# Kernel optimization log

Hardware: AMD Instinct MI355X
Metric: run time of the kernel (lower is better)

## Reference

```python
import jax, jax.numpy as jnp
import numpy as np

S0, S1 = 256, 256          # spins (up, down)
N = S0 + S1                # total electrons
SINGLE = 256               # single_dim == single_out (residual requires match)
PAIR = 128                 # pair_dim == pair_out
GAIN_TANH = 1.5927812698663017  # ActivationWithGain: 1/std(tanh(N(0,1)))
SQRT2 = 1.4142135623730951


def setup_inputs() -> dict:
    key = jax.random.key(0)
    ks = jax.random.split(key, 7)
    h_one = jax.random.normal(ks[0], (N, SINGLE), jnp.float32)
    h_two = jax.random.normal(ks[1], (N, N, PAIR), jnp.float32)
    din = SINGLE + 2 * PAIR  # one_in feature dim = 512
    # variance_scaling(2, fan_in) kernels; bias ~ Normal(0, sqrt(2))
    W1 = jax.random.normal(ks[2], (din, SINGLE), jnp.float32) * (2.0 / din) ** 0.5
    b1 = jax.random.normal(ks[3], (SINGLE,), jnp.float32) * SQRT2
    Wg = jax.random.normal(ks[4], (2 * SINGLE, SINGLE), jnp.float32) * (2.0 / (2 * SINGLE)) ** 0.5
    W2 = jax.random.normal(ks[5], (PAIR, PAIR), jnp.float32) * (2.0 / PAIR) ** 0.5
    b2 = jax.random.normal(ks[6], (PAIR,), jnp.float32) * SQRT2
    return dict(h_one=h_one, h_two=h_two, W1=W1, b1=b1, Wg=Wg, W2=W2, b2=b2)


def _act(x):
    # ActivationWithGain(tanh): rescale so output variance ~ input variance
    return jnp.tanh(x) * jnp.asarray(GAIN_TANH, x.dtype)


def reference(h_one, h_two, W1, b1, Wg, W2, b2):
    # construct_single_features: per-spin mean of h_two over sender axis
    g2_up = jnp.mean(h_two[:S0], axis=0)            # (N, PAIR)
    g2_dn = jnp.mean(h_two[S0:], axis=0)            # (N, PAIR)
    one_in = jnp.concatenate([h_one, g2_up, g2_dn], axis=1)   # (N, SINGLE+2*PAIR)
    # construct_global_features: per-spin mean of h_one, concat on features
    g1_up = jnp.mean(h_one[:S0], axis=0, keepdims=True)       # (1, SINGLE)
    g1_dn = jnp.mean(h_one[S0:], axis=0, keepdims=True)       # (1, SINGLE)
    global_in = jnp.concatenate([g1_up, g1_dn], axis=-1)      # (1, 2*SINGLE)

    h_one_new = one_in @ W1 + b1 + global_in @ Wg             # (N, SINGLE)
    h_one_new = _act(h_one_new / SQRT2)
    h_one_out = (h_one + h_one_new) / SQRT2                   # residual (shapes match)

    h_two_new = _act(h_two @ W2 + b2)                         # (N, N, PAIR)
    h_two_out = (h_two + h_two_new) / SQRT2                   # residual
    return h_one_out, h_two_out
```

## Files before the change

kernel.cpp:

```cpp
#include <hip/hip_runtime.h>
#include <stdint.h>

#define NN 512
#define PAIR 128
#define SINGLE 256

#define GAINv 1.5927812698663017f
#define RS2 0.70710678118654752f

typedef unsigned int uint;
typedef unsigned short ushort;
typedef short bf16x8 __attribute__((ext_vector_type(8)));
typedef float f32x4 __attribute__((ext_vector_type(4)));

__device__ __forceinline__ ushort f2b(float f){
  union{float f;uint i;}v; v.f=f;
  uint x=v.i;
  return (ushort)((x + 0x7FFFu + ((x>>16)&1u))>>16);
}
__device__ __forceinline__ float b2f_lo(uint u){ union{uint i;float f;}v; v.i=u<<16; return v.f; }
__device__ __forceinline__ float b2f_hi(uint u){ union{uint i;float f;}v; v.i=u&0xFFFF0000u; return v.f; }
__device__ __forceinline__ float tanh_fast(float x){
  float xc = fminf(fmaxf(x,-8.f),8.f);
  float e = __expf(2.f*xc);
  return (e-1.f)*__builtin_amdgcn_rcpf(e+1.f);
}

__global__ __launch_bounds__(256) void k1_prep(const float* __restrict__ h_one,
                                               const float* __restrict__ w2,
                                               float* __restrict__ g1part,
                                               ushort* __restrict__ wt,
                                               float* __restrict__ g2acc)
{
  const int b = blockIdx.x, t = threadIdx.x;
  if(b < 8){
    const int rb = b*64;
    float s = 0.f;
    for(int i=0;i<64;i++) s += h_one[(size_t)(rb+i)*SINGLE + t];
    g1part[b*SINGLE + t] = s;
  } else if(b < 16){
    const int bb = b-8;
    for(int e=t; e<16*128; e+=256){
      int kl = e>>7, n = e&127;
      int k = bb*16 + kl;
      wt[n*128 + k] = f2b(w2[(size_t)k*128 + n]);
    }
  } else {
    f32x4 z = (f32x4){0.f,0.f,0.f,0.f};
    f32x4* dst = (f32x4*)g2acc + (size_t)(b-16)*4096;
    for(int q=t; q<4096; q+=256) dst[q] = z;
  }
}

__global__ __launch_bounds__(256) void k2_gterm(const float* __restrict__ g1part,
                                                const float* __restrict__ wg,
                                                float* __restrict__ gtermpart)
{
  __shared__ float g1m[512];
  const int t = threadIdx.x;
  g1m[t]     = (g1part[t]      + g1part[256+t]  + g1part[512+t]  + g1part[768+t])  * (1.f/256.f);
  g1m[t+256] = (g1part[1024+t] + g1part[1280+t] + g1part[1536+t] + g1part[1792+t]) * (1.f/256.f);
  __syncthreads();
  const int fb = blockIdx.x*64;
  float s = 0.f;
  for(int f=fb; f<fb+64; f++)
    s += g1m[f]*wg[(size_t)f*SINGLE + t];
  gtermpart[blockIdx.x*SINGLE + t] = s;
}

__global__ __launch_bounds__(256, 8) void k3_htwo(
    const float* __restrict__ h_two,
    const float* __restrict__ b2,
    const ushort* __restrict__ wt,
    float* __restrict__ g2acc,
    float* __restrict__ out_h2)
{
  __shared__ __align__(16) ushort At[64*128];
  const int tid = threadIdx.x;
  const int w = tid>>6, lane = tid&63;
  const int lq = lane>>4, lr = lane&15;
  const int bi = blockIdx.x & 31, bj = blockIdx.x >> 5;
  const int i0 = bi*16, j0 = bj*4;
  const int spin = bi>>4;

  #pragma unroll
  for(int rep=0;rep<8;rep++){
    const int e = rep*1024 + tid*4;
    const int di = e>>9, c = e&511;
    const float4 v = *(const float4*)(h_two + ((size_t)(i0+di)*NN + j0)*PAIR + c);
    ushort4 pk; pk.x=f2b(v.x); pk.y=f2b(v.y); pk.z=f2b(v.z); pk.w=f2b(v.w);
    const int r = e>>7;
    *(ushort4*)(&At[e ^ ((r&7)<<3)]) = pk;
  }

  bf16x8 af[2][4];
  #pragma unroll
  for(int nt=0;nt<2;nt++){
    const int n = w*32 + nt*16 + lr;
    #pragma unroll
    for(int kk=0;kk<4;kk++)
      af[nt][kk] = *(const bf16x8*)(wt + n*128 + kk*32 + lq*8);
  }
  f32x4 bias[2];
  #pragma unroll
  for(int nt=0;nt<2;nt++){
    const float4 bv = *(const float4*)(b2 + w*32 + nt*16 + lq*4);
    bias[nt] = (f32x4){bv.x, bv.y, bv.z, bv.w};
  }
  __syncthreads();

  {
    const int dj = w, pp = lane;
    const uint* a32 = (const uint*)At;
    float s0=0.f, s1=0.f;
    #pragma unroll
    for(int di=0;di<16;di++){
      const int r = di*4+dj;
      uint u = a32[(r*64 + pp) ^ ((r&7)<<2)];
      s0 += b2f_lo(u); s1 += b2f_hi(u);
    }
    float* dst = g2acc + ((size_t)spin*NN + (j0+dj))*PAIR + pp*2;
    atomicAdd(dst, s0); atomicAdd(dst+1, s1);
  }

  f32x4 acc[4][2];
  #pragma unroll
  for(int mt=0;mt<4;mt++){
    acc[mt][0] = bias[0];
    acc[mt][1] = bias[1];
  }
  #pragma unroll
  for(int kk=0;kk<4;kk++){
    bf16x8 bfr[4];
    #pragma unroll
    for(int mt=0;mt<4;mt++){
      const int m = mt*16 + lr;
      const int e = m*128 + kk*32 + lq*8;
      bfr[mt] = *(const bf16x8*)(&At[e ^ ((lr&7)<<3)]);
    }
    #pragma unroll
    for(int mt=0;mt<4;mt++){
      acc[mt][0] = __builtin_amdgcn_mfma_f32_16x16x32_bf16(af[0][kk], bfr[mt], acc[mt][0], 0,0,0);
      acc[mt][1] = __builtin_amdgcn_mfma_f32_16x16x32_bf16(af[1][kk], bfr[mt], acc[mt][1], 0,0,0);
    }
  }

  #pragma unroll
  for(int mt=0;mt<4;mt++){
    const int m = mt*16 + lr;
    const size_t base = ((size_t)(i0 + (m>>2))*NN + (j0 + (m&3)))*PAIR;
    #pragma unroll
    for(int nt=0;nt<2;nt++){
      const int nb = w*32 + nt*16 + lq*4;
      const float4 rr = *(const float4*)(h_two + base + nb);
      f32x4 o;
      o[0] = (rr.x + GAINv*tanh_fast(acc[mt][nt][0]))*RS2;
      o[1] = (rr.y + GAINv*tanh_fast(acc[mt][nt][1]))*RS2;
      o[2] = (rr.z + GAINv*tanh_fast(acc[mt][nt][2]))*RS2;
      o[3] = (rr.w + GAINv*tanh_fast(acc[mt][nt][3]))*RS2;
      *(f32x4*)(out_h2 + base + nb) = o;
    }
  }
}

__global__ __launch_bounds__(256) void k4_hone(
    const float* __restrict__ h_one,
    const float* __restrict__ w1,
    const float* __restrict__ b1,
    const float* __restrict__ g2acc,
    const float* __restrict__ gtermpart,
    float* __restrict__ out_h1)
{
  __shared__ float onein[512];
  const int n   = threadIdx.x;
  const int row = blockIdx.x;
  onein[n] = h_one[(size_t)row*SINGLE + n];
  {
    int sp = n>>7, p = n&127;
    onein[256+n] = g2acc[((size_t)sp*NN + row)*PAIR + p] * (1.f/256.f);
  }
  float gt = 0.f;
  #pragma unroll
  for(int bb=0;bb<8;bb++) gt += gtermpart[bb*256+n];
  __syncthreads();
  float a = 0.f;
  for(int f=0; f<512; f++)
    a += onein[f] * w1[(size_t)f*SINGLE + n];
  float x = (a + b1[n] + gt) * RS2;
  out_h1[(size_t)row*SINGLE + n] = (onein[n] + GAINv*tanh_fast(x)) * RS2;
}

extern "C" void kernel_launch(void* const* d_in, const int* in_sizes, int n_in,
                              void* d_out, int out_size, void* d_ws, size_t ws_size,
                              hipStream_t stream)
{
  const float* h_one = (const float*)d_in[0];
  const float* h_two = (const float*)d_in[1];
  const float* W1    = (const float*)d_in[2];
  const float* b1    = (const float*)d_in[3];
  const float* Wg    = (const float*)d_in[4];
  const float* W2    = (const float*)d_in[5];
  const float* b2    = (const float*)d_in[6];

  float* wsf       = (float*)d_ws;
  float* g2acc     = wsf;
  ushort* wt       = (ushort*)(wsf + 131072);
  float* g1part    = wsf + 139264;
  float* gtermpart = wsf + 141312;

  float* out_h1 = (float*)d_out;
  float* out_h2 = out_h1 + 131072;

  k1_prep <<<24,   256, 0, stream>>>(h_one, W2, g1part, wt, g2acc);
  k2_gterm<<<8,    256, 0, stream>>>(g1part, Wg, gtermpart);
  k3_htwo <<<4096, 256, 0, stream>>>(h_two, b2, wt, g2acc, out_h2);
  k4_hone <<<512,  256, 0, stream>>>(h_one, W1, b1, g2acc, gtermpart, out_h1);
}
```

Baseline: 334.6 us.

## Keep h_two tile in registers for residual and stage output through LDS

The k3 kernel now holds the fp32 h_two tile it loads in registers and reuses it for the residual add, so h_two is no longer read from global memory a second time. The tanh results are transposed through LDS in two halves so output stores follow the same coalesced layout as the input loads. In exchange there are extra LDS round-trips and barriers, more registers per thread, and lower occupancy (launch bound drops from 8 to 4 blocks).

```diff
diff --git a/kernel.cpp b/kernel.cpp
--- a/kernel.cpp
+++ b/kernel.cpp
@@ -68,7 +68,7 @@
   gtermpart[blockIdx.x*SINGLE + t] = s;
 }
 
-__global__ __launch_bounds__(256, 8) void k3_htwo(
+__global__ __launch_bounds__(256, 4) void k3_htwo(
     const float* __restrict__ h_two,
     const float* __restrict__ b2,
     const ushort* __restrict__ wt,
@@ -76,6 +76,7 @@
     float* __restrict__ out_h2)
 {
   __shared__ __align__(16) ushort At[64*128];
+  float* LDSf = (float*)At;
   const int tid = threadIdx.x;
   const int w = tid>>6, lane = tid&63;
   const int lq = lane>>4, lr = lane&15;
@@ -83,13 +84,18 @@
   const int i0 = bi*16, j0 = bj*4;
   const int spin = bi>>4;
 
+  float4 L[8];
   #pragma unroll
   for(int rep=0;rep<8;rep++){
     const int e = rep*1024 + tid*4;
     const int di = e>>9, c = e&511;
-    const float4 v = *(const float4*)(h_two + ((size_t)(i0+di)*NN + j0)*PAIR + c);
-    ushort4 pk; pk.x=f2b(v.x); pk.y=f2b(v.y); pk.z=f2b(v.z); pk.w=f2b(v.w);
+    L[rep] = *(const float4*)(h_two + ((size_t)(i0+di)*NN + j0)*PAIR + c);
+  }
+  #pragma unroll
+  for(int rep=0;rep<8;rep++){
+    const int e = rep*1024 + tid*4;
     const int r = e>>7;
+    ushort4 pk; pk.x=f2b(L[rep].x); pk.y=f2b(L[rep].y); pk.z=f2b(L[rep].z); pk.w=f2b(L[rep].w);
     *(ushort4*)(&At[e ^ ((r&7)<<3)]) = pk;
   }
 
@@ -144,22 +150,42 @@
       acc[mt][1] = __builtin_amdgcn_mfma_f32_16x16x32_bf16(af[1][kk], bfr[mt], acc[mt][1], 0,0,0);
     }
   }
-
-  #pragma unroll
-  for(int mt=0;mt<4;mt++){
-    const int m = mt*16 + lr;
-    const size_t base = ((size_t)(i0 + (m>>2))*NN + (j0 + (m&3)))*PAIR;
-    #pragma unroll
-    for(int nt=0;nt<2;nt++){
-      const int nb = w*32 + nt*16 + lq*4;
-      const float4 rr = *(const float4*)(h_two + base + nb);
+  __syncthreads();
+
+  #pragma unroll
+  for(int h=0;h<2;h++){
+    #pragma unroll
+    for(int mtl=0;mtl<2;mtl++){
+      const int mt = 2*h + mtl;
+      const int rloc = (mt*16 + lr) & 31;
+      #pragma unroll
+      for(int nt=0;nt<2;nt++){
+        const int col = w*32 + nt*16 + lq*4;
+        f32x4 tv;
+        tv[0] = GAINv*tanh_fast(acc[mt][nt][0]);
+        tv[1] = GAINv*tanh_fast(acc[mt][nt][1]);
+        tv[2] = GAINv*tanh_fast(acc[mt][nt][2]);
+        tv[3] = GAINv*tanh_fast(acc[mt][nt][3]);
+        *(f32x4*)(&LDSf[rloc*128 + (col ^ ((lr&7)<<2))]) = tv;
+      }
+    }
+    __syncthreads();
+    #pragma unroll
+    for(int rep=0;rep<4;rep++){
+      const int repg = h*4 + rep;
+      const int e = repg*1024 + tid*4;
+      const int eloc = e & 4095;
+      const int r = eloc>>7, c = eloc&127;
+      const f32x4 tv = *(const f32x4*)(&LDSf[r*128 + (c ^ ((r&7)<<2))]);
+      const int di = e>>9, c511 = e&511;
       f32x4 o;
-      o[0] = (rr.x + GAINv*tanh_fast(acc[mt][nt][0]))*RS2;
-      o[1] = (rr.y + GAINv*tanh_fast(acc[mt][nt][1]))*RS2;
-      o[2] = (rr.z + GAINv*tanh_fast(acc[mt][nt][2]))*RS2;
-      o[3] = (rr.w + GAINv*tanh_fast(acc[mt][nt][3]))*RS2;
-      *(f32x4*)(out_h2 + base + nb) = o;
-    }
+      o[0] = (L[repg].x + tv[0])*RS2;
+      o[1] = (L[repg].y + tv[1])*RS2;
+      o[2] = (L[repg].z + tv[2])*RS2;
+      o[3] = (L[repg].w + tv[3])*RS2;
+      *(f32x4*)(out_h2 + ((size_t)(i0+di)*NN + j0)*PAIR + c511) = o;
+    }
+    if(h==0) __syncthreads();
   }
 }
 
```

Result: faster. 286.8 us (-14.3%).
